# Kernel tuning notes

Hardware: AMD Instinct MI355X
Metric: run time of the kernel (lower is better)

Reference implementation:

```python
import jax, jax.numpy as jnp
import numpy as np

B, H, W = 4, 256, 256
IN_HSI, IN_MSI, EMBED = 31, 3, 128
R = 2
MAX_FLOW = 2.0
REG_IN = EMBED + EMBED + (2 * R + 1) ** 2 + 1  # 282


def _conv(x, w, b=None, pad=0, groups=1):
    out = jax.lax.conv_general_dilated(
        x, w, (1, 1), [(pad, pad), (pad, pad)],
        dimension_numbers=('NCHW', 'OIHW', 'NCHW'), feature_group_count=groups)
    if b is not None:
        out = out + b[None, :, None, None]
    return out


def _gauss_window(size=9, sigma=1.5):
    c = jnp.arange(size, dtype=jnp.float32) - (size - 1) / 2.0
    g = jnp.exp(-(c ** 2) / (2.0 * sigma ** 2))
    g = g / g.sum()
    return g[:, None] * g[None, :]


def _ssim_map(a, b, win=9):
    # standard gaussian-window SSIM, per-pixel map averaged over channels
    C = a.shape[1]
    w2d = _gauss_window(win)
    k = jnp.broadcast_to(w2d[None, None], (C, 1, win, win))
    pad = win // 2
    dw = lambda t: _conv(t, k, pad=pad, groups=C)
    mu1, mu2 = dw(a), dw(b)
    mu1s, mu2s, mu12 = mu1 * mu1, mu2 * mu2, mu1 * mu2
    s1 = dw(a * a) - mu1s
    s2 = dw(b * b) - mu2s
    s12 = dw(a * b) - mu12
    C1, C2 = 0.01 ** 2, 0.03 ** 2
    m = ((2 * mu12 + C1) * (2 * s12 + C2)) / ((mu1s + mu2s + C1) * (s1 + s2 + C2))
    return m.mean(axis=1)  # (B,H,W)


def _match_mean_std(src, ref, eps=1e-6):
    sm = src.mean(axis=(2, 3), keepdims=True)
    ss = src.std(axis=(2, 3), keepdims=True, ddof=1)  # torch std is unbiased
    rm = ref.mean(axis=(2, 3), keepdims=True)
    rs = ref.std(axis=(2, 3), keepdims=True, ddof=1)
    return (src - sm) / (ss + eps) * rs + rm


def _l2norm(t, eps=1e-12):
    n = jnp.sqrt(jnp.sum(t * t, axis=1, keepdims=True))
    return t / jnp.maximum(n, eps)


def _corr_volume(q, k, r=R):
    _, _, h, w = q.shape
    q = _l2norm(q)
    k = _l2norm(k)
    kp = jnp.pad(k, ((0, 0), (0, 0), (r, r), (r, r)), mode='edge')  # replicate pad
    outs = []
    for dy in range(-r, r + 1):
        for dx in range(-r, r + 1):
            ks = kp[:, :, r + dy:r + dy + h, r + dx:r + dx + w]
            outs.append(jnp.sum(q * ks, axis=1))
    return jnp.stack(outs, axis=1)  # (B, 25, H, W)


def _reflect(coord, size):
    # PyTorch grid_sample reflection, align_corners=False: reflect about -0.5 and size-0.5
    min_ = -0.5
    span = float(size)
    c = jnp.abs(coord - min_)
    extra = jnp.mod(c, span)
    flips = jnp.floor(c / span)
    c = jnp.where(jnp.mod(flips, 2.0) == 0.0, extra + min_, span - extra + min_)
    return jnp.clip(c, 0.0, size - 1.0)


def _warp(img, flow):
    b, c, h, w = img.shape
    gx = (-1.0 + (2.0 * jnp.arange(w, dtype=img.dtype) + 1.0) / w)[None, None, :] + flow[:, 0] * (2.0 / w)
    gy = (-1.0 + (2.0 * jnp.arange(h, dtype=img.dtype) + 1.0) / h)[None, :, None] + flow[:, 1] * (2.0 / h)
    ix = _reflect(((gx + 1.0) * w - 1.0) / 2.0, w)
    iy = _reflect(((gy + 1.0) * h - 1.0) / 2.0, h)
    x0 = jnp.floor(ix)
    y0 = jnp.floor(iy)
    wx = ix - x0
    wy = iy - y0
    x0i = jnp.clip(x0.astype(jnp.int32), 0, w - 1)
    x1i = jnp.clip(x0i + 1, 0, w - 1)
    y0i = jnp.clip(y0.astype(jnp.int32), 0, h - 1)
    y1i = jnp.clip(y0i + 1, 0, h - 1)
    bi = jnp.arange(b)[:, None, None]
    g = lambda yi, xi: img[bi, :, yi, xi]  # (B,H,W,C)
    out = (g(y0i, x0i) * ((1 - wy) * (1 - wx))[..., None]
           + g(y0i, x1i) * ((1 - wy) * wx)[..., None]
           + g(y1i, x0i) * (wy * (1 - wx))[..., None]
           + g(y1i, x1i) * (wy * wx)[..., None])
    return jnp.transpose(out, (0, 3, 1, 2))


def setup_inputs() -> dict:
    key = jax.random.key(0)
    ks = jax.random.split(key, 16)

    def rn(k, shape, fan_in):
        return (jax.random.normal(k, shape, dtype=jnp.float32) / np.sqrt(fan_in)).astype(jnp.float32)

    return {
        'x': jax.random.normal(ks[0], (B, 2 * IN_HSI, H, W), dtype=jnp.float32),
        'y': jax.random.normal(ks[1], (B, IN_MSI, H, W), dtype=jnp.float32),
        'SRF': jax.random.uniform(ks[2], (IN_MSI, IN_HSI), dtype=jnp.float32) / IN_HSI,
        'conv_half_w': rn(ks[3], (IN_HSI, 2 * IN_HSI, 1, 1), 2 * IN_HSI),
        'conv_half_b': jnp.zeros((IN_HSI,), jnp.float32),
        'q_w': rn(ks[4], (EMBED, IN_HSI, 1, 1), IN_HSI),
        'q_b': jnp.zeros((EMBED,), jnp.float32),
        'k_w': rn(ks[5], (EMBED, IN_MSI, 1, 1), IN_MSI),
        'k_b': jnp.zeros((EMBED,), jnp.float32),
        'r1_w': rn(ks[6], (128, REG_IN, 3, 3), REG_IN * 9),
        'r1_b': jnp.zeros((128,), jnp.float32),
        'r2_w': rn(ks[7], (64, 128, 3, 3), 128 * 9),
        'r2_b': jnp.zeros((64,), jnp.float32),
        'r3_w': rn(ks[8], (2, 64, 1, 1), 64) * 0.1,
        'r3_b': jnp.zeros((2,), jnp.float32),
    }


def reference(x, y, SRF, conv_half_w, conv_half_b, q_w, q_b, k_w, k_b,
              r1_w, r1_b, r2_w, r2_b, r3_w, r3_b):
    x = _conv(x, conv_half_w, conv_half_b)
    x_original = x
    srf_w = SRF[:, :, None, None]  # (in_msi, in_hsi, 1, 1)
    x_projected = jnp.clip(_conv(x, srf_w), -1.0, 1.0)
    x_aligned = jnp.clip(_match_mean_std(x_projected, y), -1.0, 1.0)
    ssim_score = _ssim_map(x_aligned, y, 9)
    difficulty = jnp.clip((1.0 - ssim_score)[:, None] / 2.0, 0.0, 1.0)  # (B,1,H,W)
    q = _conv(x, q_w, q_b)
    k = _conv(y, k_w, k_b)
    corr = _corr_volume(q, k, R)
    reg_in = jnp.concatenate([q, k, corr, difficulty], axis=1)
    h1 = jax.nn.leaky_relu(_conv(reg_in, r1_w, r1_b, pad=1), 0.2)
    h2 = jax.nn.leaky_relu(_conv(h1, r2_w, r2_b, pad=1), 0.2)
    flow = jnp.tanh(_conv(h2, r3_w, r3_b)) * MAX_FLOW * difficulty
    return _warp(x_original, flow)
```

## Files before the change

### kernel.cpp

```cpp
#include <hip/hip_runtime.h>
#include <hip/hip_bf16.h>
#include <math.h>


#define HH 256
#define WWI 256
#define HW 65536
#define CH 31
#define CIN2 62
#define CM 3
#define CE 128
#define REGC 288
#define C1S 1e-4f
#define C2S 9e-4f

typedef unsigned short u16;
typedef unsigned int u32;
typedef short bf16x8 __attribute__((ext_vector_type(8)));
typedef float f32x4 __attribute__((ext_vector_type(4)));

__device__ __forceinline__ float blo(u32 u){ return __uint_as_float(u << 16); }
__device__ __forceinline__ float bhi(u32 u){ return __uint_as_float(u & 0xffff0000u); }
__device__ __forceinline__ float b1f(u16 u){ return __uint_as_float(((u32)u) << 16); }
__device__ __forceinline__ u16 f2b(float f){
    u32 u = __float_as_uint(f);
    u32 r = (u + 0x7fffu + ((u >> 16) & 1u)) >> 16;
    return (u16)r;
}
__device__ __forceinline__ f32x4 mfma16(bf16x8 a, bf16x8 b, f32x4 c){
    return __builtin_amdgcn_mfma_f32_16x16x32_bf16(a, b, c, 0, 0, 0);
}

__global__ void k_conv_half(const float* __restrict__ x, const float* __restrict__ w,
                            const float* __restrict__ bias, u16* __restrict__ x31){
    __shared__ float sw[CH*CIN2];
    __shared__ float sb[CH+1];
    for(int i=threadIdx.x;i<CH*CIN2;i+=256) sw[i]=w[i];
    for(int i=threadIdx.x;i<CH;i+=256) sb[i]=bias[i];
    __syncthreads();
    int pixg = blockIdx.x*256 + threadIdx.x;
    int b = pixg>>16, hw = pixg&65535;
    float acc[CH];
    #pragma unroll
    for(int c=0;c<CH;c++) acc[c]=sb[c];
    for(int ci=0;ci<CIN2;ci++){
        float xv = x[((size_t)(b*CIN2+ci))*HW + hw];
        #pragma unroll
        for(int c=0;c<CH;c++) acc[c] += sw[c*CIN2+ci]*xv;
    }
    u16* o = x31 + (size_t)pixg*32;
    #pragma unroll
    for(int c=0;c<CH;c++) o[c]=f2b(acc[c]);
    o[31]=0;
}

__global__ void k_project(const u16* __restrict__ x31, const float* __restrict__ srf,
                          float* __restrict__ xp){
    __shared__ float s[CM*CH];
    for(int i=threadIdx.x;i<CM*CH;i+=256) s[i]=srf[i];
    __syncthreads();
    int pixg = blockIdx.x*256 + threadIdx.x;
    int b = pixg>>16, hw = pixg&65535;
    const u16* xr = x31 + (size_t)pixg*32;
    float xv[CH];
    #pragma unroll
    for(int c=0;c<CH;c++) xv[c] = b1f(xr[c]);
    #pragma unroll
    for(int m=0;m<CM;m++){
        float acc=0.f;
        #pragma unroll
        for(int c=0;c<CH;c++) acc += s[m*CH+c]*xv[c];
        acc = fminf(fmaxf(acc,-1.f),1.f);
        xp[((size_t)(b*CM+m))*HW + hw] = acc;
    }
}

__global__ void k_stats1(const float* __restrict__ xp, const float* __restrict__ y,
                         float2* __restrict__ part, int NB){
    int bid = blockIdx.x;
    int p = bid >> 6, c = bid & 63;
    const float* src = (p<3*NB) ? (xp + (size_t)p*HW) : (y + (size_t)(p-3*NB)*HW);
    const float4* s4 = (const float4*)(src + c*1024);
    float4 v = s4[threadIdx.x];
    float s  = v.x + v.y + v.z + v.w;
    float ss = v.x*v.x + v.y*v.y + v.z*v.z + v.w*v.w;
    #pragma unroll
    for(int t=1;t<64;t<<=1){ s += __shfl_xor(s,t); ss += __shfl_xor(ss,t); }
    __shared__ float rs[4], rss[4];
    int wid = threadIdx.x>>6, lane = threadIdx.x&63;
    if(lane==0){ rs[wid]=s; rss[wid]=ss; }
    __syncthreads();
    if(threadIdx.x==0){
        part[bid] = float2{rs[0]+rs[1]+rs[2]+rs[3], rss[0]+rss[1]+rss[2]+rss[3]};
    }
}

__global__ void k_stats2(const float2* __restrict__ part, float* __restrict__ stats){
    int p = blockIdx.x;
    float2 pa = part[p*64 + threadIdx.x];
    float s = pa.x, ss = pa.y;
    #pragma unroll
    for(int t=1;t<64;t<<=1){ s += __shfl_xor(s,t); ss += __shfl_xor(ss,t); }
    if(threadIdx.x==0){
        float mean = s/(float)HW;
        float var = (ss - s*s/(float)HW) / (float)(HW-1);
        stats[p*2]   = mean;
        stats[p*2+1] = sqrtf(fmaxf(var,0.f));
    }
}

__global__ void k_align(const float* __restrict__ xp, const float* __restrict__ stats,
                        float* __restrict__ xa, int NB){
    int i = blockIdx.x*256 + threadIdx.x;
    int plane = i>>16;
    float sm = stats[plane*2], ssd = stats[plane*2+1];
    float rm = stats[(plane+3*NB)*2], rsd = stats[(plane+3*NB)*2+1];
    float v = (xp[i]-sm)/(ssd+1e-6f)*rsd + rm;
    xa[i] = fminf(fmaxf(v,-1.f),1.f);
}

__global__ void k_ssim_h(const float* __restrict__ xa, const float* __restrict__ y,
                         float* __restrict__ tmp){
    int i = blockIdx.x*256 + threadIdx.x;
    int plane = i>>16, hw = i&65535, h = hw>>8, w = hw&255;
    float g[9]; float gs=0.f;
    #pragma unroll
    for(int t=0;t<9;t++){ float cc=(float)(t-4); g[t]=expf(-cc*cc/4.5f); gs+=g[t]; }
    float inv = 1.f/gs;
    float s0=0,s1=0,s2=0,s3=0,s4=0;
    const float* xr = xa + (size_t)plane*HW + (size_t)h*256;
    const float* yr = y  + (size_t)plane*HW + (size_t)h*256;
    #pragma unroll
    for(int t=0;t<9;t++){
        int wc = w + t - 4;
        if(wc>=0 && wc<256){
            float gg = g[t]*inv;
            float a = xr[wc], b = yr[wc];
            s0+=gg*a; s1+=gg*b; s2+=gg*a*a; s3+=gg*b*b; s4+=gg*a*b;
        }
    }
    size_t base = (size_t)plane*5*HW + hw;
    tmp[base]=s0; tmp[base+HW]=s1; tmp[base+2*(size_t)HW]=s2; tmp[base+3*(size_t)HW]=s3; tmp[base+4*(size_t)HW]=s4;
}

__global__ void k_ssim_v(const float* __restrict__ tmp, float* __restrict__ diff,
                         u16* __restrict__ regin){
    int pixg = blockIdx.x*256 + threadIdx.x;
    int b = pixg>>16, hw = pixg&65535, h = hw>>8, w = hw&255;
    float g[9]; float gs=0.f;
    #pragma unroll
    for(int t=0;t<9;t++){ float cc=(float)(t-4); g[t]=expf(-cc*cc/4.5f); gs+=g[t]; }
    float inv = 1.f/gs;
    float msum = 0.f;
    for(int m=0;m<3;m++){
        int plane = b*3+m;
        float v0=0,v1=0,v2=0,v3=0,v4=0;
        #pragma unroll
        for(int t=0;t<9;t++){
            int hc = h + t - 4;
            if(hc>=0 && hc<256){
                float gg = g[t]*inv;
                size_t base = (size_t)plane*5*HW + (size_t)hc*256 + w;
                v0+=gg*tmp[base]; v1+=gg*tmp[base+HW]; v2+=gg*tmp[base+2*(size_t)HW];
                v3+=gg*tmp[base+3*(size_t)HW]; v4+=gg*tmp[base+4*(size_t)HW];
            }
        }
        float mu1=v0, mu2=v1;
        float mu1s=mu1*mu1, mu2s=mu2*mu2, mu12=mu1*mu2;
        float sg1=v2-mu1s, sg2=v3-mu2s, sg12=v4-mu12;
        float num=(2.f*mu12+C1S)*(2.f*sg12+C2S);
        float den=(mu1s+mu2s+C1S)*(sg1+sg2+C2S);
        msum += num/den;
    }
    float ss = msum*(1.f/3.f);
    float d = fminf(fmaxf((1.f-ss)*0.5f,0.f),1.f);
    diff[pixg] = d;
    regin[(size_t)pixg*REGC + 281] = f2b(d);
}

__global__ __launch_bounds__(128) void k_qk(const u16* __restrict__ x31,
                     const float* __restrict__ y,
                     const float* __restrict__ qw, const float* __restrict__ qb,
                     const float* __restrict__ kw, const float* __restrict__ kb,
                     u16* __restrict__ regin){
    __shared__ float sqw[CE*CH];
    __shared__ float skw[CE*CM];
    __shared__ float sqb[CE], skb[CE];
    for(int i=threadIdx.x;i<CE*CH;i+=128) sqw[i]=qw[i];
    for(int i=threadIdx.x;i<CE*CM;i+=128) skw[i]=kw[i];
    if(threadIdx.x<CE){ sqb[threadIdx.x]=qb[threadIdx.x]; skb[threadIdx.x]=kb[threadIdx.x]; }
    __syncthreads();
    int co = threadIdx.x;
    int p0 = blockIdx.x*32;
    float wk0 = skw[co*CM+0], wk1 = skw[co*CM+1], wk2 = skw[co*CM+2];
    for(int pp=0;pp<32;pp++){
        int pixg = p0+pp;
        int b = pixg>>16, hw = pixg&65535;
        const u16* xr = x31 + (size_t)pixg*32;
        float acc = sqb[co];
        #pragma unroll
        for(int c=0;c<CH;c++) acc += sqw[co*CH+c]*b1f(xr[c]);
        u16* rg = regin + (size_t)pixg*REGC;
        rg[co] = f2b(acc);
        float ack = skb[co] + wk0*y[((size_t)(b*CM  ))*HW+hw]
                            + wk1*y[((size_t)(b*CM+1))*HW+hw]
                            + wk2*y[((size_t)(b*CM+2))*HW+hw];
        rg[128+co] = f2b(ack);
        if(co<6) rg[282+co] = 0;
    }
}

__global__ __launch_bounds__(256) void k_norms(const u16* __restrict__ regin,
                                               float* __restrict__ qinv,
                                               float* __restrict__ kinv){
    int t = threadIdx.x;
    int half = t & 1, pidx = t >> 1;
    int pixg = blockIdx.x*128 + pidx;
    const uint4* qp = (const uint4*)(regin + (size_t)pixg*REGC) + half*8;
    const uint4* kp = (const uint4*)(regin + (size_t)pixg*REGC + 128) + half*8;
    float sq = 0.f, sk = 0.f;
    #pragma unroll
    for(int i=0;i<8;i++){
        uint4 v = qp[i];
        sq += blo(v.x)*blo(v.x) + bhi(v.x)*bhi(v.x) + blo(v.y)*blo(v.y) + bhi(v.y)*bhi(v.y)
            + blo(v.z)*blo(v.z) + bhi(v.z)*bhi(v.z) + blo(v.w)*blo(v.w) + bhi(v.w)*bhi(v.w);
    }
    #pragma unroll
    for(int i=0;i<8;i++){
        uint4 v = kp[i];
        sk += blo(v.x)*blo(v.x) + bhi(v.x)*bhi(v.x) + blo(v.y)*blo(v.y) + bhi(v.y)*bhi(v.y)
            + blo(v.z)*blo(v.z) + bhi(v.z)*bhi(v.z) + blo(v.w)*blo(v.w) + bhi(v.w)*bhi(v.w);
    }
    sq += __shfl_xor(sq, 1);
    sk += __shfl_xor(sk, 1);
    if(half==0){
        qinv[pixg] = 1.f/fmaxf(sqrtf(sq),1e-12f);
        kinv[pixg] = 1.f/fmaxf(sqrtf(sk),1e-12f);
    }
}

__global__ __launch_bounds__(512) void k_corr(const u16* __restrict__ regin,
                                              const float* __restrict__ qinv,
                                              const float* __restrict__ kinv,
                                              u16* __restrict__ regout){
    __shared__ uint4 klv[432*16];
    __shared__ float kinvl[432];
    int t = threadIdx.x;
    int half = t & 1, pidx = t >> 1;
    int bid = blockIdx.x;
    int bb = bid >> 8;
    int s2 = bid & 255;
    int tx = s2 & 7, ty = s2 >> 3;
    int lw = pidx & 31, lh = pidx >> 5;
    int w = tx*32 + lw;
    int h = ty*8 + lh;
    int pixg = (bb<<16) + (h<<8) + w;

    for(int s = t; s < 432*16; s += 512){
        int rpx = s >> 4, g = s & 15;
        int rr = rpx/36, cc = rpx - rr*36;
        int gy = min(max(ty*8-2+rr,0),255);
        int gx = min(max(tx*32-2+cc,0),255);
        const uint4* src = (const uint4*)(regin + ((size_t)((bb<<16)+(gy<<8)+gx))*REGC + 128);
        klv[rpx*16 + (g ^ (rpx&15))] = src[g];
    }
    if(t < 432){
        int rr = t/36, cc = t - rr*36;
        int gy = min(max(ty*8-2+rr,0),255);
        int gx = min(max(tx*32-2+cc,0),255);
        kinvl[t] = kinv[(bb<<16)+(gy<<8)+gx];
    }
    __syncthreads();

    uint4 q[8];
    const uint4* qp = (const uint4*)(regin + (size_t)pixg*REGC) + half*8;
    #pragma unroll
    for(int i=0;i<8;i++) q[i] = qp[i];
    float qn = qinv[pixg];

    float res[13];
    #pragma unroll
    for(int dy=-2;dy<=2;dy++){
        #pragma unroll
        for(int dx=-2;dx<=2;dx++){
            int rpx = (lh+2+dy)*36 + (lw+2+dx);
            const uint4* kp = &klv[rpx*16];
            int sw = rpx & 15;
            float s = 0.f;
            #pragma unroll
            for(int i=0;i<8;i++){
                uint4 kv = kp[(half*8 + i) ^ sw];
                uint4 qv = q[i];
                s += blo(qv.x)*blo(kv.x) + bhi(qv.x)*bhi(kv.x);
                s += blo(qv.y)*blo(kv.y) + bhi(qv.y)*bhi(kv.y);
                s += blo(qv.z)*blo(kv.z) + bhi(qv.z)*bhi(kv.z);
                s += blo(qv.w)*blo(kv.w) + bhi(qv.w)*bhi(kv.w);
            }
            s += __shfl_xor(s, 1);
            float cv = s*qn*kinvl[rpx];
            int o = (dy+2)*5 + (dx+2);
            if(o < 13){ if(half==0) res[o] = cv; }
            else      { if(half==1) res[o-13] = cv; }
        }
    }

    u16* rg = regout + (size_t)pixg*REGC + 256;
    if(half==0){
        u16 p[13];
        #pragma unroll
        for(int i=0;i<13;i++) p[i] = f2b(res[i]);
        uint4 v0; u32* v0p = (u32*)&v0;
        #pragma unroll
        for(int i=0;i<4;i++) v0p[i] = (u32)p[2*i] | ((u32)p[2*i+1]<<16);
        *(uint4*)(rg) = v0;
        *(u32*)(rg+8)  = (u32)p[8]  | ((u32)p[9]<<16);
        *(u32*)(rg+10) = (u32)p[10] | ((u32)p[11]<<16);
        rg[12] = p[12];
    } else {
        u16 p[12];
        #pragma unroll
        for(int i=0;i<12;i++) p[i] = f2b(res[i]);
        rg[13] = p[0];
        *(u32*)(rg+14) = (u32)p[1] | ((u32)p[2]<<16);
        uint4 v1; u32* v1p = (u32*)&v1;
        #pragma unroll
        for(int i=0;i<4;i++) v1p[i] = (u32)p[3+2*i] | ((u32)p[4+2*i]<<16);
        *(uint4*)(rg+16) = v1;
        rg[24] = p[11];
    }
}

__global__ void k_wre(const float* __restrict__ w1, const float* __restrict__ w2,
                      u16* __restrict__ w1f, u16* __restrict__ w2f,
                      u16* __restrict__ zpad){
    int i = blockIdx.x*256 + threadIdx.x;
    if(i < 32) zpad[i] = 0;
    if(i < 9*9*128*32){
        int j = i & 7;
        int gg = (i>>3)&3;
        int co = (i>>5)&127;
        int rest = i>>12;
        int kbg = rest%9, tap = rest/9;
        int ci = kbg*32 + gg*8 + j;
        float v = (ci<282) ? w1[((size_t)co*282 + ci)*9 + tap] : 0.f;
        w1f[i] = f2b(v);
    }
    if(i < 9*4*64*32){
        int j = i & 7;
        int gg = (i>>3)&3;
        int co = (i>>5)&63;
        int rest = i>>11;
        int kbg = rest&3, tap = rest>>2;
        int ci = kbg*32 + gg*8 + j;
        w2f[i] = f2b(w2[((size_t)co*128 + ci)*9 + tap]);
    }
}

template<int MF>
__device__ __forceinline__ void ldaM(const uint4* sbuf, int ky, int kx, int kb,
                                     int lane15, int lgrp, bf16x8* ar){
    #pragma unroll
    for(int mf=0;mf<MF;mf++){
        int spx  = (mf&1)*16 + lane15 + kx;
        int srow = (mf>>1) + ky;
        int slot = (srow*34 + spx)*8 + ((kb*4 + lgrp) ^ (spx&7));
        ar[mf] = *(const bf16x8*)&sbuf[slot];
    }
}

template<int NF, int KBGT, int NCO>
__device__ __forceinline__ void ldbN(const u16* __restrict__ wf, int kbg, int tap,
                                     int co0, int lane15, int lgrp, bf16x8* br){
    #pragma unroll
    for(int nf=0;nf<NF;nf++){
        size_t idx = ((size_t)((tap*KBGT + kbg)*NCO + co0 + nf*16 + lane15))*4 + lgrp;
        br[nf] = *(const bf16x8*)(wf + idx*8);
    }
}

template<int MF, int NF, int KBGT, int NCO, int KBI>
__device__ __forceinline__ void conv_steps(const uint4* sbuf, const u16* __restrict__ wf,
                                           int kbgbase, int co0, int lane15, int lgrp,
                                           f32x4 (&acc)[MF][NF]){
    constexpr int NST = 9*KBI;
    #pragma unroll
    for(int s=0;s<NST;s++){
        int ky,kx,kb;
        if(KBI==2){ ky = s/6; kx = (s>>1)%3; kb = s&1; }
        else      { ky = s/3; kx = s%3;      kb = 0;   }
        bf16x8 a[MF];
        bf16x8 b[NF];
        ldaM<MF>(sbuf, ky,kx,kb, lane15, lgrp, a);
        ldbN<NF,KBGT,NCO>(wf, kbgbase+kb, ky*3+kx, co0, lane15, lgrp, b);
        #pragma unroll
        for(int mf=0;mf<MF;mf++)
            #pragma unroll
            for(int nf=0;nf<NF;nf++)
                acc[mf][nf] = mfma16(a[mf], b[nf], acc[mf][nf]);
    }
}

template<int CSTRIDE, int CINTOT, int NCO, int KBGT, int TM>
__global__ __launch_bounds__(128, 1) void k_conv3(const u16* __restrict__ in,
                                                  const u16* __restrict__ wf,
                                                  const float* __restrict__ bias,
                                                  u16* __restrict__ out,
                                                  const u16* __restrict__ zpad){
    constexpr int NW = 2;
    constexpr int NF = NCO/(16*NW);
    constexpr int MF = 2*TM;
    constexpr int NCHUNK = (CINTOT + 63)/64;
    constexpr int NTH = NW*64;
    constexpr int SLOTS = (TM+2)*34*8;
    __shared__ uint4 sT[2*SLOTS];
    int t = threadIdx.x;
    int lane15 = t & 15, lgrp = (t >> 4) & 3;
    int co0 = (t >> 6) * (NCO/NW);
    int rb = blockIdx.x;
    int bid = (rb & 7)*(gridDim.x >> 3) + (rb >> 3);
    int bb = bid >> 9;
    int s2 = bid & 511;
    int tx = s2 & 7, ty = s2 >> 3;
    int row0 = ty*TM, col0 = tx*32;
    const u16* inb  = in  + (size_t)bb*HW*CSTRIDE;
    u16*       outb = out + (size_t)bb*HW*NCO;

    f32x4 acc[MF][NF];
    #pragma unroll
    for(int nf=0;nf<NF;nf++){
        float bsv = bias[co0 + nf*16 + lane15];
        #pragma unroll
        for(int mf=0;mf<MF;mf++) acc[mf][nf] = f32x4{bsv,bsv,bsv,bsv};
    }

    auto stage = [&](int buf, int kc){
        constexpr int NIT = (SLOTS + NTH - 1)/NTH;
        #pragma unroll
        for(int it=0; it<NIT; ++it){
            int s = it*NTH + t;
            if(s >= SLOTS) continue;
            int srow = s/272, rem = s - srow*272;
            int spx = rem>>3, ggp = rem&7;
            int gg = ggp ^ (spx&7);
            int gy = row0-1+srow, gx = col0-1+spx;
            bool ok = ((unsigned)gy<256u) && ((unsigned)gx<256u);
            const u16* src = ok ? (inb + (size_t)((gy<<8)+gx)*CSTRIDE + kc + gg*8) : zpad;
            __builtin_amdgcn_global_load_lds(
                (const __attribute__((address_space(1))) u32*)src,
                (__attribute__((address_space(3))) u32*)&sT[buf*SLOTS + s],
                16, 0, 0);
        }
    };

    stage(0, 0);
    __syncthreads();

    int cur = 0;
    for(int j=0;j<NCHUNK;j++){
        if(j+1 < NCHUNK) stage(cur^1, (j+1)*64);
        if(CINTOT==288 && j==NCHUNK-1)
            conv_steps<MF,NF,KBGT,NCO,1>(&sT[cur*SLOTS], wf, j*2, co0, lane15, lgrp, acc);
        else
            conv_steps<MF,NF,KBGT,NCO,2>(&sT[cur*SLOTS], wf, j*2, co0, lane15, lgrp, acc);
        if(j+1 < NCHUNK){
            __syncthreads();
            cur ^= 1;
        }
    }

    #pragma unroll
    for(int mf=0;mf<MF;mf++){
        int prow  = row0 + (mf>>1);
        int pcolb = col0 + (mf&1)*16 + lgrp*4;
        #pragma unroll
        for(int nf=0;nf<NF;nf++){
            int co = co0 + nf*16 + lane15;
            #pragma unroll
            for(int r=0;r<4;r++){
                int pix = (prow<<8) + pcolb + r;
                float v = acc[mf][nf][r];
                v = (v>0.f) ? v : 0.2f*v;
                outb[(size_t)pix*NCO + co] = f2b(v);
            }
        }
    }
}

__device__ __forceinline__ float reflectc(float coord, float size){
    float c = fabsf(coord + 0.5f);
    float extra = fmodf(c, size);
    float flips = floorf(c/size);
    float fo = fmodf(flips, 2.0f);
    float r = (fo == 0.0f) ? (extra - 0.5f) : (size - extra - 0.5f);
    return fminf(fmaxf(r, 0.0f), size - 1.0f);
}

__global__ void k_flowwarp(const u16* __restrict__ h2, const float* __restrict__ w3,
                           const float* __restrict__ b3, const float* __restrict__ diff,
                           const u16* __restrict__ x31, float* __restrict__ out){
    __shared__ float sw[130];
    for(int i=threadIdx.x;i<128;i+=256) sw[i]=w3[i];
    if(threadIdx.x<2) sw[128+threadIdx.x]=b3[threadIdx.x];
    __syncthreads();
    int pixg = blockIdx.x*256 + threadIdx.x;
    int b = pixg>>16, hw = pixg&65535, h = hw>>8, w = hw&255;
    const uint4* h4 = (const uint4*)(h2 + (size_t)pixg*64);
    float f0 = sw[128], f1 = sw[129];
    #pragma unroll
    for(int cc=0;cc<8;cc++){
        uint4 u = h4[cc];
        float vv[8] = {blo(u.x),bhi(u.x),blo(u.y),bhi(u.y),blo(u.z),bhi(u.z),blo(u.w),bhi(u.w)};
        #pragma unroll
        for(int j=0;j<8;j++){ int c = cc*8+j; f0 += sw[c]*vv[j]; f1 += sw[64+c]*vv[j]; }
    }
    float d = diff[pixg];
    f0 = tanhf(f0)*2.0f*d;
    f1 = tanhf(f1)*2.0f*d;
    float ix = reflectc((float)w + f0, 256.f);
    float iy = reflectc((float)h + f1, 256.f);
    float x0 = floorf(ix), y0 = floorf(iy);
    float wx = ix-x0, wy = iy-y0;
    int x0i = min(max((int)x0,0),255);
    int x1i = min(x0i+1,255);
    int y0i = min(max((int)y0,0),255);
    int y1i = min(y0i+1,255);
    const u16* p00 = x31 + ((size_t)((b<<16)+(y0i<<8)+x0i))*32;
    const u16* p01 = x31 + ((size_t)((b<<16)+(y0i<<8)+x1i))*32;
    const u16* p10 = x31 + ((size_t)((b<<16)+(y1i<<8)+x0i))*32;
    const u16* p11 = x31 + ((size_t)((b<<16)+(y1i<<8)+x1i))*32;
    float w00=(1.f-wy)*(1.f-wx), w01=(1.f-wy)*wx, w10=wy*(1.f-wx), w11=wy*wx;
    float* ob = out + (size_t)b*CH*HW + hw;
    #pragma unroll
    for(int c=0;c<CH;c++){
        ob[(size_t)c*HW] = w00*b1f(p00[c]) + w01*b1f(p01[c])
                         + w10*b1f(p10[c]) + w11*b1f(p11[c]);
    }
}

extern "C" void kernel_launch(void* const* d_in, const int* in_sizes, int n_in,
                              void* d_out, int out_size, void* d_ws, size_t ws_size,
                              hipStream_t stream) {
    const float* x    = (const float*)d_in[0];
    const float* y    = (const float*)d_in[1];
    const float* srf  = (const float*)d_in[2];
    const float* chw  = (const float*)d_in[3];
    const float* chb  = (const float*)d_in[4];
    const float* qw   = (const float*)d_in[5];
    const float* qb   = (const float*)d_in[6];
    const float* kw   = (const float*)d_in[7];
    const float* kb   = (const float*)d_in[8];
    const float* w1   = (const float*)d_in[9];
    const float* b1p  = (const float*)d_in[10];
    const float* w2   = (const float*)d_in[11];
    const float* b2p  = (const float*)d_in[12];
    const float* w3   = (const float*)d_in[13];
    const float* b3p  = (const float*)d_in[14];

    struct Arena {
        u16 *x31, *regin, *h1, *h2, *w1f, *w2f, *zpad;
        float *xp, *xa, *stats, *diff, *qinv, *kinv, *tmp;
        float2 *part;
    };
    auto layout = [&](char* base, int G, Arena* A)->size_t{
        size_t o = 0;
        auto take = [&](size_t sz)->char*{ char* p = base ? base+o : 0; o += (sz+255)&~255ull; return p; };
        if(A){
            A->x31   = (u16*)  take((size_t)G*HW*32*2);
            A->xp    = (float*)take((size_t)G*3*HW*4);
            A->stats = (float*)take(6*4*2*4);
            A->part  = (float2*)take((size_t)6*4*64*8);
            A->diff  = (float*)take((size_t)G*HW*4);
            A->qinv  = (float*)take((size_t)G*HW*4);
            A->kinv  = (float*)take((size_t)G*HW*4);
            A->regin = (u16*)  take((size_t)G*HW*REGC*2);
            A->w1f   = (u16*)  take((size_t)9*9*128*32*2);
            A->w2f   = (u16*)  take((size_t)9*4*64*32*2);
            A->zpad  = (u16*)  take(64);
            size_t uo = o;
            A->xa    = (float*)take((size_t)G*3*HW*4);
            A->tmp   = (float*)take((size_t)G*15*HW*4);
            size_t frontEnd = o;
            o = uo;
            A->h1    = (u16*)  take((size_t)G*HW*128*2);
            A->h2    = (u16*)  take((size_t)G*HW*64*2);
            if(frontEnd > o) o = frontEnd;
        } else {
            take((size_t)G*HW*32*2); take((size_t)G*3*HW*4); take(6*4*2*4);
            take((size_t)6*4*64*8); take((size_t)G*HW*4); take((size_t)G*HW*4);
            take((size_t)G*HW*4); take((size_t)G*HW*REGC*2);
            take((size_t)9*9*128*32*2); take((size_t)9*4*64*32*2); take(64);
            size_t uo = o;
            take((size_t)G*3*HW*4); take((size_t)G*15*HW*4);
            size_t frontEnd = o; o = uo;
            take((size_t)G*HW*128*2); take((size_t)G*HW*64*2);
            if(frontEnd > o) o = frontEnd;
        }
        return o;
    };

    int G = 4;
    while(G > 1 && layout(nullptr, G, nullptr) > ws_size) G >>= 1;
    Arena A;
    layout((char*)d_ws, G, &A);

    k_wre<<<1296, 256, 0, stream>>>(w1, w2, A.w1f, A.w2f, A.zpad);

    for(int g0=0; g0<4; g0+=G){
        int NB = G;
        const float* xg  = x + (size_t)g0*CIN2*HW;
        const float* yg  = y + (size_t)g0*CM*HW;
        float* outg      = (float*)d_out + (size_t)g0*CH*HW;

        k_conv_half<<<NB*256,  256, 0, stream>>>(xg, chw, chb, A.x31);
        k_project  <<<NB*256,  256, 0, stream>>>(A.x31, srf, A.xp);
        k_stats1   <<<NB*384,  256, 0, stream>>>(A.xp, yg, A.part, NB);
        k_stats2   <<<NB*6,     64, 0, stream>>>(A.part, A.stats);
        k_align    <<<NB*768,  256, 0, stream>>>(A.xp, A.stats, A.xa, NB);
        k_ssim_h   <<<NB*768,  256, 0, stream>>>(A.xa, yg, A.tmp);
        k_ssim_v   <<<NB*256,  256, 0, stream>>>(A.tmp, A.diff, A.regin);
        k_qk       <<<NB*2048, 128, 0, stream>>>(A.x31, yg, qw, qb, kw, kb, A.regin);
        k_norms    <<<NB*512,  256, 0, stream>>>(A.regin, A.qinv, A.kinv);
        k_corr     <<<NB*256,  512, 0, stream>>>(A.regin, A.qinv, A.kinv, A.regin);
        k_conv3<288,288,128,9,4><<<NB*512, 128, 0, stream>>>(A.regin, A.w1f, b1p, A.h1, A.zpad);
        k_conv3<128,128, 64,4,4><<<NB*512, 128, 0, stream>>>(A.h1, A.w2f, b2p, A.h2, A.zpad);
        k_flowwarp <<<NB*256,  256, 0, stream>>>(A.h2, w3, b3p, A.diff, A.x31, outg);
    }
}
```

Before: 731.5 us.

## Fuse align and separable SSIM into one tiled kernel; fold norms into corr

Replaces the align, horizontal SSIM and vertical SSIM kernels with a single 32x32-tiled kernel that normalizes, blurs horizontally and vertically in shared memory, so the 15-plane temporary buffer and aligned-image buffer are no longer written and read through global memory. The separate q/k norm kernel is removed: k_corr computes key inverse norms from its shared halo tile and query norms from registers already loaded. The workspace layout is simplified by dropping the now-unused buffers. The fused SSIM kernel launches only 256 blocks and recomputes halo values, which may limit occupancy, and corr does extra redundant norm work per tile.

```diff
diff --git a/kernel.cpp b/kernel.cpp
--- a/kernel.cpp
+++ b/kernel.cpp
@@ -109,73 +109,94 @@
     }
 }
 
-__global__ void k_align(const float* __restrict__ xp, const float* __restrict__ stats,
-                        float* __restrict__ xa, int NB){
-    int i = blockIdx.x*256 + threadIdx.x;
-    int plane = i>>16;
-    float sm = stats[plane*2], ssd = stats[plane*2+1];
-    float rm = stats[(plane+3*NB)*2], rsd = stats[(plane+3*NB)*2+1];
-    float v = (xp[i]-sm)/(ssd+1e-6f)*rsd + rm;
-    xa[i] = fminf(fmaxf(v,-1.f),1.f);
-}
-
-__global__ void k_ssim_h(const float* __restrict__ xa, const float* __restrict__ y,
-                         float* __restrict__ tmp){
-    int i = blockIdx.x*256 + threadIdx.x;
-    int plane = i>>16, hw = i&65535, h = hw>>8, w = hw&255;
-    float g[9]; float gs=0.f;
-    #pragma unroll
-    for(int t=0;t<9;t++){ float cc=(float)(t-4); g[t]=expf(-cc*cc/4.5f); gs+=g[t]; }
-    float inv = 1.f/gs;
-    float s0=0,s1=0,s2=0,s3=0,s4=0;
-    const float* xr = xa + (size_t)plane*HW + (size_t)h*256;
-    const float* yr = y  + (size_t)plane*HW + (size_t)h*256;
-    #pragma unroll
-    for(int t=0;t<9;t++){
-        int wc = w + t - 4;
-        if(wc>=0 && wc<256){
-            float gg = g[t]*inv;
-            float a = xr[wc], b = yr[wc];
-            s0+=gg*a; s1+=gg*b; s2+=gg*a*a; s3+=gg*b*b; s4+=gg*a*b;
-        }
-    }
-    size_t base = (size_t)plane*5*HW + hw;
-    tmp[base]=s0; tmp[base+HW]=s1; tmp[base+2*(size_t)HW]=s2; tmp[base+3*(size_t)HW]=s3; tmp[base+4*(size_t)HW]=s4;
-}
-
-__global__ void k_ssim_v(const float* __restrict__ tmp, float* __restrict__ diff,
-                         u16* __restrict__ regin){
-    int pixg = blockIdx.x*256 + threadIdx.x;
-    int b = pixg>>16, hw = pixg&65535, h = hw>>8, w = hw&255;
-    float g[9]; float gs=0.f;
-    #pragma unroll
-    for(int t=0;t<9;t++){ float cc=(float)(t-4); g[t]=expf(-cc*cc/4.5f); gs+=g[t]; }
-    float inv = 1.f/gs;
-    float msum = 0.f;
+__global__ __launch_bounds__(256) void k_ssim(const float* __restrict__ xp,
+                                              const float* __restrict__ y,
+                                              const float* __restrict__ stats,
+                                              float* __restrict__ diff,
+                                              u16* __restrict__ regin, int NB){
+    __shared__ float sxa[1600];
+    __shared__ float sy2[1600];
+    __shared__ float hs[5][1280];
+    int t = threadIdx.x;
+    int bid = blockIdx.x;
+    int bb = bid >> 6;
+    int s2 = bid & 63;
+    int tx = s2 & 7, ty = s2 >> 3;
+    float g[9]; float gs = 0.f;
+    #pragma unroll
+    for(int k=0;k<9;k++){ float cc=(float)(k-4); g[k]=expf(-cc*cc/4.5f); gs+=g[k]; }
+    float ginv = 1.f/gs;
+    #pragma unroll
+    for(int k=0;k<9;k++) g[k] *= ginv;
+
+    float msum[4] = {0.f,0.f,0.f,0.f};
     for(int m=0;m<3;m++){
-        int plane = b*3+m;
-        float v0=0,v1=0,v2=0,v3=0,v4=0;
-        #pragma unroll
-        for(int t=0;t<9;t++){
-            int hc = h + t - 4;
-            if(hc>=0 && hc<256){
-                float gg = g[t]*inv;
-                size_t base = (size_t)plane*5*HW + (size_t)hc*256 + w;
-                v0+=gg*tmp[base]; v1+=gg*tmp[base+HW]; v2+=gg*tmp[base+2*(size_t)HW];
-                v3+=gg*tmp[base+3*(size_t)HW]; v4+=gg*tmp[base+4*(size_t)HW];
+        int plane = bb*3+m;
+        float sm = stats[plane*2],        ssd = stats[plane*2+1];
+        float rm = stats[(plane+3*NB)*2], rsd = stats[(plane+3*NB)*2+1];
+        const float* xpp = xp + (size_t)plane*HW;
+        const float* yp  = y  + (size_t)plane*HW;
+        if(m) __syncthreads();
+        #pragma unroll
+        for(int it=0; it<7; ++it){
+            int s = it*256 + t;
+            if(s < 1600){
+                int rr = s/40, cc = s - rr*40;
+                int gy = ty*32-4+rr, gx = tx*32-4+cc;
+                float xv=0.f, yv=0.f;
+                if(((unsigned)gy<256u)&&((unsigned)gx<256u)){
+                    float v = xpp[(gy<<8)+gx];
+                    v = (v-sm)/(ssd+1e-6f)*rsd + rm;
+                    xv = fminf(fmaxf(v,-1.f),1.f);
+                    yv = yp[(gy<<8)+gx];
+                }
+                sxa[s]=xv; sy2[s]=yv;
             }
         }
-        float mu1=v0, mu2=v1;
-        float mu1s=mu1*mu1, mu2s=mu2*mu2, mu12=mu1*mu2;
-        float sg1=v2-mu1s, sg2=v3-mu2s, sg12=v4-mu12;
-        float num=(2.f*mu12+C1S)*(2.f*sg12+C2S);
-        float den=(mu1s+mu2s+C1S)*(sg1+sg2+C2S);
-        msum += num/den;
-    }
-    float ss = msum*(1.f/3.f);
-    float d = fminf(fmaxf((1.f-ss)*0.5f,0.f),1.f);
-    diff[pixg] = d;
-    regin[(size_t)pixg*REGC + 281] = f2b(d);
+        __syncthreads();
+        #pragma unroll
+        for(int it=0; it<5; ++it){
+            int s = it*256 + t;
+            int rr = s>>5, cc = s&31;
+            int base = rr*40 + cc;
+            float s0=0,s1=0,s2v=0,s3=0,s4=0;
+            #pragma unroll
+            for(int k=0;k<9;k++){
+                float gg=g[k];
+                float a=sxa[base+k], b=sy2[base+k];
+                s0+=gg*a; s1+=gg*b; s2v+=gg*a*a; s3+=gg*b*b; s4+=gg*a*b;
+            }
+            hs[0][s]=s0; hs[1][s]=s1; hs[2][s]=s2v; hs[3][s]=s3; hs[4][s]=s4;
+        }
+        __syncthreads();
+        #pragma unroll
+        for(int it=0; it<4; ++it){
+            int s = it*256 + t;
+            int rr = s>>5, cc = s&31;
+            float v0=0,v1=0,v2=0,v3=0,v4=0;
+            #pragma unroll
+            for(int k=0;k<9;k++){
+                float gg=g[k];
+                int idx=(rr+k)*32+cc;
+                v0+=gg*hs[0][idx]; v1+=gg*hs[1][idx]; v2+=gg*hs[2][idx];
+                v3+=gg*hs[3][idx]; v4+=gg*hs[4][idx];
+            }
+            float mu1=v0, mu2=v1;
+            float mu1s=mu1*mu1, mu2s=mu2*mu2, mu12=mu1*mu2;
+            float sg1=v2-mu1s, sg2=v3-mu2s, sg12=v4-mu12;
+            msum[it] += (2.f*mu12+C1S)*(2.f*sg12+C2S)
+                      / ((mu1s+mu2s+C1S)*(sg1+sg2+C2S));
+        }
+    }
+    #pragma unroll
+    for(int it=0; it<4; ++it){
+        int s = it*256 + t;
+        int rr = s>>5, cc = s&31;
+        int pixg = (bb<<16) + ((ty*32+rr)<<8) + (tx*32+cc);
+        float d = fminf(fmaxf((1.f-msum[it]*(1.f/3.f))*0.5f,0.f),1.f);
+        diff[pixg] = d;
+        regin[(size_t)pixg*REGC + 281] = f2b(d);
+    }
 }
 
 __global__ __launch_bounds__(128) void k_qk(const u16* __restrict__ x31,
@@ -210,38 +231,7 @@
     }
 }
 
-__global__ __launch_bounds__(256) void k_norms(const u16* __restrict__ regin,
-                                               float* __restrict__ qinv,
-                                               float* __restrict__ kinv){
-    int t = threadIdx.x;
-    int half = t & 1, pidx = t >> 1;
-    int pixg = blockIdx.x*128 + pidx;
-    const uint4* qp = (const uint4*)(regin + (size_t)pixg*REGC) + half*8;
-    const uint4* kp = (const uint4*)(regin + (size_t)pixg*REGC + 128) + half*8;
-    float sq = 0.f, sk = 0.f;
-    #pragma unroll
-    for(int i=0;i<8;i++){
-        uint4 v = qp[i];
-        sq += blo(v.x)*blo(v.x) + bhi(v.x)*bhi(v.x) + blo(v.y)*blo(v.y) + bhi(v.y)*bhi(v.y)
-            + blo(v.z)*blo(v.z) + bhi(v.z)*bhi(v.z) + blo(v.w)*blo(v.w) + bhi(v.w)*bhi(v.w);
-    }
-    #pragma unroll
-    for(int i=0;i<8;i++){
-        uint4 v = kp[i];
-        sk += blo(v.x)*blo(v.x) + bhi(v.x)*bhi(v.x) + blo(v.y)*blo(v.y) + bhi(v.y)*bhi(v.y)
-            + blo(v.z)*blo(v.z) + bhi(v.z)*bhi(v.z) + blo(v.w)*blo(v.w) + bhi(v.w)*bhi(v.w);
-    }
-    sq += __shfl_xor(sq, 1);
-    sk += __shfl_xor(sk, 1);
-    if(half==0){
-        qinv[pixg] = 1.f/fmaxf(sqrtf(sq),1e-12f);
-        kinv[pixg] = 1.f/fmaxf(sqrtf(sk),1e-12f);
-    }
-}
-
 __global__ __launch_bounds__(512) void k_corr(const u16* __restrict__ regin,
-                                              const float* __restrict__ qinv,
-                                              const float* __restrict__ kinv,
                                               u16* __restrict__ regout){
     __shared__ uint4 klv[432*16];
     __shared__ float kinvl[432];
@@ -264,11 +254,27 @@
         const uint4* src = (const uint4*)(regin + ((size_t)((bb<<16)+(gy<<8)+gx))*REGC + 128);
         klv[rpx*16 + (g ^ (rpx&15))] = src[g];
     }
-    if(t < 432){
-        int rr = t/36, cc = t - rr*36;
-        int gy = min(max(ty*8-2+rr,0),255);
-        int gx = min(max(tx*32-2+cc,0),255);
-        kinvl[t] = kinv[(bb<<16)+(gy<<8)+gx];
+    __syncthreads();
+
+    #pragma unroll
+    for(int it=0; it<2; ++it){
+        int item = it*512 + t;
+        int px = item>>1, hf = item&1;
+        float s = 0.f;
+        if(item < 864){
+            const uint4* kp = &klv[px*16];
+            int sw = px & 15;
+            #pragma unroll
+            for(int i=0;i<8;i++){
+                uint4 kv = kp[(hf*8+i)^sw];
+                s += blo(kv.x)*blo(kv.x)+bhi(kv.x)*bhi(kv.x)
+                   + blo(kv.y)*blo(kv.y)+bhi(kv.y)*bhi(kv.y)
+                   + blo(kv.z)*blo(kv.z)+bhi(kv.z)*bhi(kv.z)
+                   + blo(kv.w)*blo(kv.w)+bhi(kv.w)*bhi(kv.w);
+            }
+        }
+        float so = s + __shfl_xor(s,1);
+        if(item < 864 && hf==0) kinvl[px] = 1.f/fmaxf(sqrtf(so),1e-12f);
     }
     __syncthreads();
 
@@ -276,7 +282,15 @@
     const uint4* qp = (const uint4*)(regin + (size_t)pixg*REGC) + half*8;
     #pragma unroll
     for(int i=0;i<8;i++) q[i] = qp[i];
-    float qn = qinv[pixg];
+    float sq = 0.f;
+    #pragma unroll
+    for(int i=0;i<8;i++){
+        uint4 v = q[i];
+        sq += blo(v.x)*blo(v.x)+bhi(v.x)*bhi(v.x) + blo(v.y)*blo(v.y)+bhi(v.y)*bhi(v.y)
+            + blo(v.z)*blo(v.z)+bhi(v.z)*bhi(v.z) + blo(v.w)*blo(v.w)+bhi(v.w)*bhi(v.w);
+    }
+    sq += __shfl_xor(sq, 1);
+    float qn = 1.f/fmaxf(sqrtf(sq),1e-12f);
 
     float res[13];
     #pragma unroll
@@ -558,43 +572,24 @@
 
     struct Arena {
         u16 *x31, *regin, *h1, *h2, *w1f, *w2f, *zpad;
-        float *xp, *xa, *stats, *diff, *qinv, *kinv, *tmp;
+        float *xp, *stats, *diff;
         float2 *part;
     };
     auto layout = [&](char* base, int G, Arena* A)->size_t{
         size_t o = 0;
         auto take = [&](size_t sz)->char*{ char* p = base ? base+o : 0; o += (sz+255)&~255ull; return p; };
-        if(A){
-            A->x31   = (u16*)  take((size_t)G*HW*32*2);
-            A->xp    = (float*)take((size_t)G*3*HW*4);
-            A->stats = (float*)take(6*4*2*4);
-            A->part  = (float2*)take((size_t)6*4*64*8);
-            A->diff  = (float*)take((size_t)G*HW*4);
-            A->qinv  = (float*)take((size_t)G*HW*4);
-            A->kinv  = (float*)take((size_t)G*HW*4);
-            A->regin = (u16*)  take((size_t)G*HW*REGC*2);
-            A->w1f   = (u16*)  take((size_t)9*9*128*32*2);
-            A->w2f   = (u16*)  take((size_t)9*4*64*32*2);
-            A->zpad  = (u16*)  take(64);
-            size_t uo = o;
-            A->xa    = (float*)take((size_t)G*3*HW*4);
-            A->tmp   = (float*)take((size_t)G*15*HW*4);
-            size_t frontEnd = o;
-            o = uo;
-            A->h1    = (u16*)  take((size_t)G*HW*128*2);
-            A->h2    = (u16*)  take((size_t)G*HW*64*2);
-            if(frontEnd > o) o = frontEnd;
-        } else {
-            take((size_t)G*HW*32*2); take((size_t)G*3*HW*4); take(6*4*2*4);
-            take((size_t)6*4*64*8); take((size_t)G*HW*4); take((size_t)G*HW*4);
-            take((size_t)G*HW*4); take((size_t)G*HW*REGC*2);
-            take((size_t)9*9*128*32*2); take((size_t)9*4*64*32*2); take(64);
-            size_t uo = o;
-            take((size_t)G*3*HW*4); take((size_t)G*15*HW*4);
-            size_t frontEnd = o; o = uo;
-            take((size_t)G*HW*128*2); take((size_t)G*HW*64*2);
-            if(frontEnd > o) o = frontEnd;
-        }
+        Arena tmpA; Arena* P = A ? A : &tmpA;
+        P->x31   = (u16*)  take((size_t)G*HW*32*2);
+        P->xp    = (float*)take((size_t)G*3*HW*4);
+        P->stats = (float*)take(6*4*2*4);
+        P->part  = (float2*)take((size_t)6*4*64*8);
+        P->diff  = (float*)take((size_t)G*HW*4);
+        P->regin = (u16*)  take((size_t)G*HW*REGC*2);
+        P->h1    = (u16*)  take((size_t)G*HW*128*2);
+        P->h2    = (u16*)  take((size_t)G*HW*64*2);
+        P->w1f   = (u16*)  take((size_t)9*9*128*32*2);
+        P->w2f   = (u16*)  take((size_t)9*4*64*32*2);
+        P->zpad  = (u16*)  take(64);
         return o;
     };
 
@@ -615,12 +610,9 @@
         k_project  <<<NB*256,  256, 0, stream>>>(A.x31, srf, A.xp);
         k_stats1   <<<NB*384,  256, 0, stream>>>(A.xp, yg, A.part, NB);
         k_stats2   <<<NB*6,     64, 0, stream>>>(A.part, A.stats);
-        k_align    <<<NB*768,  256, 0, stream>>>(A.xp, A.stats, A.xa, NB);
-        k_ssim_h   <<<NB*768,  256, 0, stream>>>(A.xa, yg, A.tmp);
-        k_ssim_v   <<<NB*256,  256, 0, stream>>>(A.tmp, A.diff, A.regin);
+        k_ssim     <<<NB*64,   256, 0, stream>>>(A.xp, yg, A.stats, A.diff, A.regin, NB);
         k_qk       <<<NB*2048, 128, 0, stream>>>(A.x31, yg, qw, qb, kw, kb, A.regin);
-        k_norms    <<<NB*512,  256, 0, stream>>>(A.regin, A.qinv, A.kinv);
-        k_corr     <<<NB*256,  512, 0, stream>>>(A.regin, A.qinv, A.kinv, A.regin);
+        k_corr     <<<NB*256,  512, 0, stream>>>(A.regin, A.regin);
         k_conv3<288,288,128,9,4><<<NB*512, 128, 0, stream>>>(A.regin, A.w1f, b1p, A.h1, A.zpad);
         k_conv3<128,128, 64,4,4><<<NB*512, 128, 0, stream>>>(A.h1, A.w2f, b2p, A.h2, A.zpad);
         k_flowwarp <<<NB*256,  256, 0, stream>>>(A.h2, w3, b3p, A.diff, A.x31, outg);
```

After: 690.8 us. 1.06x faster.
